# Performance work log

Hardware: AMD Instinct MI355X
Metric: run time of the kernel (lower is better)

## Reference

```python
import jax, jax.numpy as jnp
import numpy as np

B, H, W = 4, 512, 512
CIN, COUT = 3, 3
K = CIN + COUT  # 6x6 per-pixel Gaussian covariance factors


def setup_inputs() -> dict:
    key = jax.random.key(0)
    ks = jax.random.split(key, 6)
    x = jax.random.normal(ks[0], (B, CIN, H, W), jnp.float32)
    y = jax.random.normal(ks[1], (B, COUT, H, W), jnp.float32)
    m = jax.random.normal(ks[2], (B, K, H, W), jnp.float32)
    S = jax.random.normal(ks[3], (B, H, W, K, K), jnp.float32)
    I = jnp.eye(K, dtype=jnp.float32)
    # well-conditioned factors so linalg.inv is stable
    R = I + 0.1 * jax.random.normal(ks[4], (B, H, W, K, K), jnp.float32)
    D = 2.0 * I + 0.1 * jax.random.normal(ks[5], (B, H, W, K, K), jnp.float32)
    return {"x": x, "y": y, "m": m, "S": S, "R": R, "D": D}


def reference(x, y, m, S, R, D):
    C = CIN
    # get_my_by_x: S^{-1} = R D^{-1} R^T, per-pixel 6x6
    D_1 = jnp.linalg.inv(D)                      # [B,H,W,K,K]
    RT = jnp.swapaxes(R, -1, -2)
    S_1 = R @ D_1 @ RT                           # [B,H,W,K,K]
    Sxx = S_1[..., :C, :C]
    Syx = S_1[..., C:, :C]
    Q = Syx @ jnp.linalg.inv(Sxx)                # [B,H,W,COUT,CIN]
    mx = m[:, :C]
    my = m[:, C:]
    y_ = my + jnp.einsum('bijmn,bnij->bmij', Q, x - mx)  # [B,COUT,H,W]
    # reflect first 3 coords in the R-basis
    z = jnp.concatenate([x, y_], axis=1) - m     # [B,K,H,W]
    z = jnp.einsum('bmij,bijmn->bnij', z, RT)
    z = z.at[:, :3].multiply(-1.0)               # hardcoded :3 as in source
    z = jnp.einsum('bmij,bijmn->bnij', z, R) + m
    x_ = z[:, :3]
    y_out = z[:, 3:]
    S_out = jnp.transpose(S, (0, 3, 4, 1, 2))    # [B,K,K,H,W]
    return (x_, y_out, m, S_out)
```

## Files before the change

kernel.cpp:

```cpp
#include <hip/hip_runtime.h>

#define HWC (512 * 512)
#define BATCH 4
#define NPIX (BATCH * HWC)

__global__ __launch_bounds__(256) void gpenc_math(
    const float* __restrict__ x,
    const float* __restrict__ m,
    const float* __restrict__ R,
    const float* __restrict__ Dm,
    float* __restrict__ xout,
    float* __restrict__ yout,
    float* __restrict__ mout)
{
    const int g = blockIdx.x * 256 + threadIdx.x;
    const int b = g >> 18;
    const int p = g & (HWC - 1);

    float d[36], r[36];
    {
        const float4* D4 = reinterpret_cast<const float4*>(Dm + (size_t)g * 36);
        const float4* R4 = reinterpret_cast<const float4*>(R  + (size_t)g * 36);
#pragma unroll
        for (int i = 0; i < 9; ++i) {
            float4 v = D4[i];
            d[4*i+0] = v.x; d[4*i+1] = v.y; d[4*i+2] = v.z; d[4*i+3] = v.w;
            float4 w = R4[i];
            r[4*i+0] = w.x; r[4*i+1] = w.y; r[4*i+2] = w.z; r[4*i+3] = w.w;
        }
    }

    const size_t xb = (size_t)b * 3 * HWC + p;
    const size_t mb = (size_t)b * 6 * HWC + p;
    float xv[3], mv[6];
#pragma unroll
    for (int c = 0; c < 3; ++c) xv[c] = x[xb + (size_t)c * HWC];
#pragma unroll
    for (int c = 0; c < 6; ++c) mv[c] = m[mb + (size_t)c * HWC];

    float rdiag[6];
#pragma unroll
    for (int k = 0; k < 6; ++k) {
        rdiag[k] = 1.0f / d[k*6 + k];
#pragma unroll
        for (int i = k + 1; i < 6; ++i) {
            float l = d[i*6 + k] * rdiag[k];
            d[i*6 + k] = l;
#pragma unroll
            for (int j = k + 1; j < 6; ++j) d[i*6 + j] -= l * d[k*6 + j];
        }
    }

    float X[18];
#pragma unroll
    for (int c = 0; c < 3; ++c) {
        float t[6];
#pragma unroll
        for (int i = 0; i < 6; ++i) {
            float s = r[c*6 + i];
#pragma unroll
            for (int j = 0; j < i; ++j) s -= d[i*6 + j] * t[j];
            t[i] = s;
        }
#pragma unroll
        for (int i = 5; i >= 0; --i) {
            float s = t[i];
#pragma unroll
            for (int j = i + 1; j < 6; ++j) s -= d[i*6 + j] * t[j];
            t[i] = s * rdiag[i];
        }
#pragma unroll
        for (int i = 0; i < 6; ++i) X[i*3 + c] = t[i];
    }

    float s1[18];
#pragma unroll
    for (int i = 0; i < 6; ++i) {
#pragma unroll
        for (int c = 0; c < 3; ++c) {
            float s = 0.0f;
#pragma unroll
            for (int j = 0; j < 6; ++j) s += r[i*6 + j] * X[j*3 + c];
            s1[i*3 + c] = s;
        }
    }

    const float a00 = s1[0], a01 = s1[1], a02 = s1[2];
    const float a10 = s1[3], a11 = s1[4], a12 = s1[5];
    const float a20 = s1[6], a21 = s1[7], a22 = s1[8];
    const float c00 =  (a11*a22 - a12*a21);
    const float c01 = -(a10*a22 - a12*a20);
    const float c02 =  (a10*a21 - a11*a20);
    const float det = a00*c00 + a01*c01 + a02*c02;
    const float rdet = 1.0f / det;
    float iS[9];
    iS[0] = c00 * rdet;
    iS[1] = -(a01*a22 - a02*a21) * rdet;
    iS[2] =  (a01*a12 - a02*a11) * rdet;
    iS[3] = c01 * rdet;
    iS[4] =  (a00*a22 - a02*a20) * rdet;
    iS[5] = -(a00*a12 - a02*a10) * rdet;
    iS[6] = c02 * rdet;
    iS[7] = -(a00*a21 - a01*a20) * rdet;
    iS[8] =  (a00*a11 - a01*a10) * rdet;

    float Q[9];
#pragma unroll
    for (int mm = 0; mm < 3; ++mm) {
#pragma unroll
        for (int n = 0; n < 3; ++n) {
            float s = 0.0f;
#pragma unroll
            for (int k = 0; k < 3; ++k) s += s1[(3 + mm)*3 + k] * iS[k*3 + n];
            Q[mm*3 + n] = s;
        }
    }

    float z[6];
#pragma unroll
    for (int n = 0; n < 3; ++n) z[n] = xv[n] - mv[n];
#pragma unroll
    for (int mm = 0; mm < 3; ++mm) {
        float s = 0.0f;
#pragma unroll
        for (int n = 0; n < 3; ++n) s += Q[mm*3 + n] * z[n];
        z[3 + mm] = s;
    }

    float z1[6];
#pragma unroll
    for (int n = 0; n < 6; ++n) {
        float s = 0.0f;
#pragma unroll
        for (int mm = 0; mm < 6; ++mm) s += r[n*6 + mm] * z[mm];
        z1[n] = (n < 3) ? -s : s;
    }
    float z2[6];
#pragma unroll
    for (int n = 0; n < 6; ++n) {
        float s = 0.0f;
#pragma unroll
        for (int mm = 0; mm < 6; ++mm) s += z1[mm] * r[mm*6 + n];
        z2[n] = s + mv[n];
    }

#pragma unroll
    for (int c = 0; c < 3; ++c) xout[xb + (size_t)c * HWC] = z2[c];
#pragma unroll
    for (int c = 0; c < 3; ++c) yout[xb + (size_t)c * HWC] = z2[3 + c];
#pragma unroll
    for (int c = 0; c < 6; ++c) mout[mb + (size_t)c * HWC] = mv[c];
}

__global__ __launch_bounds__(256) void gpenc_transpose(
    const float* __restrict__ S,
    float* __restrict__ Sout)
{
    const int g = blockIdx.x * 256 + threadIdx.x;
    const int b = g >> 18;
    const int p = g & (HWC - 1);
    const float4* S4 = reinterpret_cast<const float4*>(S + (size_t)g * 36);
    float* out = Sout + (size_t)b * 36 * HWC + p;
#pragma unroll
    for (int i = 0; i < 9; ++i) {
        float4 v = S4[i];
        out[(size_t)(4*i + 0) * HWC] = v.x;
        out[(size_t)(4*i + 1) * HWC] = v.y;
        out[(size_t)(4*i + 2) * HWC] = v.z;
        out[(size_t)(4*i + 3) * HWC] = v.w;
    }
}

extern "C" void kernel_launch(void* const* d_in, const int* in_sizes, int n_in,
                              void* d_out, int out_size, void* d_ws, size_t ws_size,
                              hipStream_t stream) {
    const float* x  = (const float*)d_in[0];
    const float* m  = (const float*)d_in[2];
    const float* S  = (const float*)d_in[3];
    const float* R  = (const float*)d_in[4];
    const float* D  = (const float*)d_in[5];

    float* out = (float*)d_out;
    const size_t N3 = (size_t)BATCH * 3 * HWC;
    const size_t N6 = (size_t)BATCH * 6 * HWC;
    float* xout = out;
    float* yout = out + N3;
    float* mout = out + 2 * N3;
    float* Sout = out + 2 * N3 + N6;

    const int threads = 256;
    const int blocks = NPIX / threads;

    gpenc_math<<<blocks, threads, 0, stream>>>(x, m, R, D, xout, yout, mout);
    gpenc_transpose<<<blocks, threads, 0, stream>>>(S, Sout);
}
```

Baseline: 166.6 us.

## Stage per-pixel D and R loads through LDS for coalesced global reads

Each wave now loads its 64 pixels' D and R matrices as contiguous float4 chunks, so consecutive lanes read consecutive addresses. The data is then transposed through a per-wave shared-memory buffer so each thread gets its own 36-element matrix. The previous per-thread 144-byte strided float4 loads were poorly coalesced. It also sets launch_bounds occupancy to 4 blocks per CU, and in exchange adds LDS traffic, block-wide barriers and 36 KB of shared memory per block, which may itself limit occupancy.

```diff
diff --git a/kernel.cpp b/kernel.cpp
--- a/kernel.cpp
+++ b/kernel.cpp
@@ -4,7 +4,7 @@
 #define BATCH 4
 #define NPIX (BATCH * HWC)
 
-__global__ __launch_bounds__(256) void gpenc_math(
+__global__ __launch_bounds__(256, 4) void gpenc_math(
     const float* __restrict__ x,
     const float* __restrict__ m,
     const float* __restrict__ R,
@@ -13,22 +13,26 @@
     float* __restrict__ yout,
     float* __restrict__ mout)
 {
-    const int g = blockIdx.x * 256 + threadIdx.x;
+    __shared__ float4 lbuf[4 * 576];
+
+    const int t = threadIdx.x;
+    const int w = t >> 6;
+    const int l = t & 63;
+    const int g = blockIdx.x * 256 + t;
     const int b = g >> 18;
     const int p = g & (HWC - 1);
 
-    float d[36], r[36];
-    {
-        const float4* D4 = reinterpret_cast<const float4*>(Dm + (size_t)g * 36);
-        const float4* R4 = reinterpret_cast<const float4*>(R  + (size_t)g * 36);
-#pragma unroll
-        for (int i = 0; i < 9; ++i) {
-            float4 v = D4[i];
-            d[4*i+0] = v.x; d[4*i+1] = v.y; d[4*i+2] = v.z; d[4*i+3] = v.w;
-            float4 w = R4[i];
-            r[4*i+0] = w.x; r[4*i+1] = w.y; r[4*i+2] = w.z; r[4*i+3] = w.w;
-        }
-    }
+    float4* wbuf = lbuf + w * 576;
+    const size_t waveBase4 = ((size_t)blockIdx.x * 256 + (size_t)w * 64) * 9;
+
+    const float4* D4 = reinterpret_cast<const float4*>(Dm);
+    const float4* R4 = reinterpret_cast<const float4*>(R);
+
+    float4 sd[9], sr[9];
+#pragma unroll
+    for (int i = 0; i < 9; ++i) sd[i] = D4[waveBase4 + (size_t)(i * 64 + l)];
+#pragma unroll
+    for (int i = 0; i < 9; ++i) sr[i] = R4[waveBase4 + (size_t)(i * 64 + l)];
 
     const size_t xb = (size_t)b * 3 * HWC + p;
     const size_t mb = (size_t)b * 6 * HWC + p;
@@ -38,39 +42,61 @@
 #pragma unroll
     for (int c = 0; c < 6; ++c) mv[c] = m[mb + (size_t)c * HWC];
 
+#pragma unroll
+    for (int i = 0; i < 9; ++i) wbuf[i * 64 + l] = sd[i];
+    __syncthreads();
+    float d[36];
+#pragma unroll
+    for (int i = 0; i < 9; ++i) {
+        float4 v = wbuf[l * 9 + i];
+        d[4*i+0] = v.x; d[4*i+1] = v.y; d[4*i+2] = v.z; d[4*i+3] = v.w;
+    }
+    __syncthreads();
+
+#pragma unroll
+    for (int i = 0; i < 9; ++i) wbuf[i * 64 + l] = sr[i];
+
     float rdiag[6];
 #pragma unroll
     for (int k = 0; k < 6; ++k) {
         rdiag[k] = 1.0f / d[k*6 + k];
 #pragma unroll
         for (int i = k + 1; i < 6; ++i) {
-            float l = d[i*6 + k] * rdiag[k];
-            d[i*6 + k] = l;
-#pragma unroll
-            for (int j = k + 1; j < 6; ++j) d[i*6 + j] -= l * d[k*6 + j];
-        }
+            float lo = d[i*6 + k] * rdiag[k];
+            d[i*6 + k] = lo;
+#pragma unroll
+            for (int j = k + 1; j < 6; ++j) d[i*6 + j] -= lo * d[k*6 + j];
+        }
+    }
+
+    __syncthreads();
+    float r[36];
+#pragma unroll
+    for (int i = 0; i < 9; ++i) {
+        float4 v = wbuf[l * 9 + i];
+        r[4*i+0] = v.x; r[4*i+1] = v.y; r[4*i+2] = v.z; r[4*i+3] = v.w;
     }
 
     float X[18];
 #pragma unroll
     for (int c = 0; c < 3; ++c) {
-        float t[6];
+        float tt[6];
 #pragma unroll
         for (int i = 0; i < 6; ++i) {
             float s = r[c*6 + i];
 #pragma unroll
-            for (int j = 0; j < i; ++j) s -= d[i*6 + j] * t[j];
-            t[i] = s;
+            for (int j = 0; j < i; ++j) s -= d[i*6 + j] * tt[j];
+            tt[i] = s;
         }
 #pragma unroll
         for (int i = 5; i >= 0; --i) {
-            float s = t[i];
-#pragma unroll
-            for (int j = i + 1; j < 6; ++j) s -= d[i*6 + j] * t[j];
-            t[i] = s * rdiag[i];
-        }
-#pragma unroll
-        for (int i = 0; i < 6; ++i) X[i*3 + c] = t[i];
+            float s = tt[i];
+#pragma unroll
+            for (int j = i + 1; j < 6; ++j) s -= d[i*6 + j] * tt[j];
+            tt[i] = s * rdiag[i];
+        }
+#pragma unroll
+        for (int i = 0; i < 6; ++i) X[i*3 + c] = tt[i];
     }
 
     float s1[18];
```

Measured after the change: 174.8 us. +4.9%, slower.
